# Performance work log

Hardware: AMD Instinct MI355X
Metric: run time of the kernel (lower is better)

Reference implementation:

```python
import jax, jax.numpy as jnp
import numpy as np

B, T, D = 4, 2048, 1024
H, S = 16, 64  # n_heads, stalk_dim; D == H*S
P_ADIC_BASE = 2
MAX_VAL = 16


def quantize_6bit(x):
    # symmetric int6 quantization with straight-through estimator
    scale = jnp.max(jnp.abs(x)) / 31.0 + 1e-8
    q = jnp.clip(jnp.round(x / scale), -31, 31) * scale
    return x + jax.lax.stop_gradient(q - x)


def build_p_adic_bias(seq_len, p=2, max_val=16):
    idx = jnp.arange(seq_len)
    d = jnp.abs(idx[:, None] - idx[None, :])
    nonzero = d > 0
    vp = jnp.zeros_like(d)
    work = d
    for _ in range(max_val):  # fixed iterations; v_2(|i-j|) <= log2(T) < 16
        divisible = nonzero & (work % p == 0)
        vp = vp + divisible.astype(vp.dtype)
        work = jnp.where(divisible, work // p, work)
    vals = jnp.minimum(vp, max_val).astype(jnp.float32)
    vals = jnp.where(nonzero, vals, jnp.float32(max_val))
    return vals / max_val


def setup_inputs() -> dict:
    key = jax.random.key(0)
    ks = jax.random.split(key, 8)
    std = 0.02
    return {
        "x": jax.random.normal(ks[0], (B, T, D), dtype=jnp.float32),
        "wq": jax.random.normal(ks[1], (D, D), dtype=jnp.float32) * std,
        "wk": jax.random.normal(ks[2], (D, D), dtype=jnp.float32) * std,
        "wv": jax.random.normal(ks[3], (D, D), dtype=jnp.float32) * std,
        "wo": jax.random.normal(ks[4], (D, D), dtype=jnp.float32) * std,
        "wu": jax.random.normal(ks[5], (S, S), dtype=jnp.float32) * std,
        "wsv": jax.random.normal(ks[6], (S, S), dtype=jnp.float32) * std,
        "p_scale": jnp.ones((1,), dtype=jnp.float32) * 0.1,
    }


def reference(x, wq, wk, wv, wo, wu, wsv, p_scale):
    h, s = H, S
    scale = 1.0 / jnp.sqrt(jnp.float32(s))
    # quantized linear projections (F.linear: x @ W.T)
    Q = (x @ quantize_6bit(wq).T).reshape(B, T, h, s).transpose(0, 2, 1, 3)
    K = (x @ quantize_6bit(wk).T).reshape(B, T, h, s).transpose(0, 2, 1, 3)
    V = (x @ quantize_6bit(wv).T).reshape(B, T, h, s).transpose(0, 2, 1, 3)
    # stalk (low-rank sheaf) maps on the head dim
    Qs = Q @ quantize_6bit(wu).T
    Ks = K @ quantize_6bit(wsv).T
    scores = jnp.einsum("bhqs,bhks->bhqk", Qs, Ks) * scale
    p_bias = build_p_adic_bias(T, p=P_ADIC_BASE, max_val=MAX_VAL)
    scores = scores + p_scale[0] * p_bias[None, None, :, :]
    causal = jnp.triu(jnp.ones((T, T), dtype=bool), k=1)
    scores = jnp.where(causal[None, None], -jnp.inf, scores)
    attn = jax.nn.softmax(scores, axis=-1)
    out = jnp.einsum("bhqk,bhks->bhqs", attn, V)
    out = out.transpose(0, 2, 1, 3).reshape(B, T, D)
    return out @ quantize_6bit(wo).T
```

## Files before the change

### kernel.cpp

```cpp
#include <hip/hip_runtime.h>
#include <hip/hip_bf16.h>
#include <stdint.h>


typedef __bf16 bf16_t;
typedef __attribute__((ext_vector_type(8))) __bf16 bf16x8;
typedef __attribute__((ext_vector_type(4))) float f32x4;

#define BB 4
#define TT 2048
#define DD 1024
#define HH 16
#define SS 64

__device__ __forceinline__ float quant6(float v, float s) {
    float q = rintf(v / s);
    q = fminf(fmaxf(q, -31.0f), 31.0f);
    return q * s;
}

__device__ __forceinline__ float fexp2(float x) {
#if __has_builtin(__builtin_amdgcn_exp2f)
    return __builtin_amdgcn_exp2f(x);
#else
    return exp2f(x);
#endif
}

typedef __attribute__((address_space(3))) uint32_t lds_u32;
typedef const __attribute__((address_space(1))) uint32_t glb_u32;

__global__ __launch_bounds__(256) void absmax6(const float* __restrict__ wq,
                                               const float* __restrict__ wk,
                                               const float* __restrict__ wv,
                                               const float* __restrict__ wo,
                                               const float* __restrict__ wu,
                                               const float* __restrict__ wsv,
                                               float* __restrict__ amax) {
    const int t = blockIdx.y;
    const float* src = (t == 0) ? wq : (t == 1) ? wk : (t == 2) ? wv
                     : (t == 3) ? wo : (t == 4) ? wu : wsv;
    const int n4 = (t < 4) ? (1048576 / 4) : (4096 / 4);
    float m = 0.0f;
    for (int i = blockIdx.x * blockDim.x + threadIdx.x; i < n4; i += gridDim.x * blockDim.x) {
        float4 v = ((const float4*)src)[i];
        m = fmaxf(m, fmaxf(fmaxf(fabsf(v.x), fabsf(v.y)), fmaxf(fabsf(v.z), fabsf(v.w))));
    }
    #pragma unroll
    for (int mask = 32; mask > 0; mask >>= 1)
        m = fmaxf(m, __shfl_xor(m, mask));
    __shared__ float red[4];
    int w = threadIdx.x >> 6;
    if ((threadIdx.x & 63) == 0) red[w] = m;
    __syncthreads();
    if (threadIdx.x == 0) {
        m = fmaxf(fmaxf(red[0], red[1]), fmaxf(red[2], red[3]));
        atomicMax((int*)(amax + t), __float_as_int(m));
    }
}

__global__ __launch_bounds__(256) void xcvt_kernel(const float* __restrict__ x,
                                                   bf16_t* __restrict__ xb) {
    int i = (blockIdx.x * 256 + threadIdx.x) * 8;
    float4 f0 = *(const float4*)(x + i);
    float4 f1 = *(const float4*)(x + i + 4);
    bf16x8 v;
    v[0] = (bf16_t)f0.x; v[1] = (bf16_t)f0.y; v[2] = (bf16_t)f0.z; v[3] = (bf16_t)f0.w;
    v[4] = (bf16_t)f1.x; v[5] = (bf16_t)f1.y; v[6] = (bf16_t)f1.z; v[7] = (bf16_t)f1.w;
    *(bf16x8*)(xb + i) = v;
}

__global__ __launch_bounds__(256) void quant_cast2(const float* __restrict__ wv,
                                                   const float* __restrict__ wo,
                                                   const float* __restrict__ amax,
                                                   bf16_t* __restrict__ dv,
                                                   bf16_t* __restrict__ dw) {
    const int which = blockIdx.y;
    const float* src = which ? wo : wv;
    bf16_t* dst = which ? dw : dv;
    float s = amax[which ? 3 : 2] / 31.0f + 1e-8f;
    int i = (blockIdx.x * 256 + threadIdx.x) * 8;
    float4 f0 = *(const float4*)(src + i);
    float4 f1 = *(const float4*)(src + i + 4);
    bf16x8 v;
    v[0] = (bf16_t)quant6(f0.x, s); v[1] = (bf16_t)quant6(f0.y, s);
    v[2] = (bf16_t)quant6(f0.z, s); v[3] = (bf16_t)quant6(f0.w, s);
    v[4] = (bf16_t)quant6(f1.x, s); v[5] = (bf16_t)quant6(f1.y, s);
    v[6] = (bf16_t)quant6(f1.z, s); v[7] = (bf16_t)quant6(f1.w, s);
    *(bf16x8*)(dst + i) = v;
}

__global__ __launch_bounds__(256) void fold_mfma(const float* __restrict__ wq,
                                                 const float* __restrict__ wk,
                                                 const float* __restrict__ wu,
                                                 const float* __restrict__ wsv,
                                                 const float* __restrict__ amax,
                                                 bf16_t* __restrict__ W_all) {
    const int which = blockIdx.y;
    const float* wbig = which ? wk : wq;
    const float* wsml = which ? wsv : wu;
    const float sb = amax[which ? 1 : 0] / 31.0f + 1e-8f;
    const float ss = amax[which ? 5 : 4] / 31.0f + 1e-8f;
    const float oscale = which ? 1.0f : 0.125f * 1.44269504089f;
    bf16_t* outp = W_all + (size_t)which * 1024 * 1024;
    const int h = blockIdx.x >> 4, n0 = (blockIdx.x & 15) * 64;
    const int w = threadIdx.x >> 6, l = threadIdx.x & 63;
    const int l15 = l & 15, quad = l >> 4, q8 = quad * 8;
    const int m0 = w * 16;

    bf16x8 af[2];
    #pragma unroll
    for (int kc = 0; kc < 2; ++kc) {
        const float* src = wsml + (m0 + l15) * 64 + kc * 32 + q8;
        float4 f0 = *(const float4*)(src);
        float4 f1 = *(const float4*)(src + 4);
        bf16x8 a;
        a[0] = (bf16_t)quant6(f0.x, ss); a[1] = (bf16_t)quant6(f0.y, ss);
        a[2] = (bf16_t)quant6(f0.z, ss); a[3] = (bf16_t)quant6(f0.w, ss);
        a[4] = (bf16_t)quant6(f1.x, ss); a[5] = (bf16_t)quant6(f1.y, ss);
        a[6] = (bf16_t)quant6(f1.z, ss); a[7] = (bf16_t)quant6(f1.w, ss);
        af[kc] = a;
    }
    f32x4 acc[4];
    #pragma unroll
    for (int nb = 0; nb < 4; ++nb) acc[nb] = (f32x4){0.f, 0.f, 0.f, 0.f};
    #pragma unroll
    for (int kc = 0; kc < 2; ++kc) {
        #pragma unroll
        for (int nb = 0; nb < 4; ++nb) {
            bf16x8 bfr;
            #pragma unroll
            for (int j = 0; j < 8; ++j)
                bfr[j] = (bf16_t)quant6(wbig[(size_t)(h * 64 + kc * 32 + q8 + j) * 1024 + n0 + nb * 16 + l15], sb);
            acc[nb] = __builtin_amdgcn_mfma_f32_16x16x32_bf16(af[kc], bfr, acc[nb], 0, 0, 0);
        }
    }
    #pragma unroll
    for (int nb = 0; nb < 4; ++nb)
        #pragma unroll
        for (int r = 0; r < 4; ++r)
            outp[(size_t)(h * 64 + m0 + quad * 4 + r) * 1024 + n0 + nb * 16 + l15] =
                (bf16_t)(acc[nb][r] * oscale);
}

template <bool OUT_F32>
__global__ __launch_bounds__(256) void gemm128(const bf16_t* __restrict__ A,
                                               const bf16_t* __restrict__ Bt,
                                               void* __restrict__ Cv,
                                               int lda, int ldb, int ldc, int K) {
    __shared__ __align__(16) bf16_t As[128 * 64];
    __shared__ __align__(16) bf16_t Bs[128 * 64];
    const int tid = threadIdx.x;
    const int w = tid >> 6, l = tid & 63;
    const int l15 = l & 15, quad = l >> 4;
    const int m0 = blockIdx.y * 128, n0 = blockIdx.x * 128;
    const int wm = (w & 1) * 64, wn = (w >> 1) * 64;

    f32x4 acc[4][4];
    #pragma unroll
    for (int a = 0; a < 4; ++a)
        #pragma unroll
        for (int b = 0; b < 4; ++b) acc[a][b] = (f32x4){0.f, 0.f, 0.f, 0.f};

    for (int kc = 0; kc < K; kc += 64) {
        __syncthreads();
        #pragma unroll
        for (int rep = 0; rep < 4; ++rep) {
            int ci = rep * 256 + w * 64 + l;
            int row = ci >> 3, slot = ci & 7;
            int gch = slot ^ ((row ^ (row >> 3)) & 7);
            __builtin_amdgcn_global_load_lds(
                (glb_u32*)(A + (size_t)(m0 + row) * lda + kc + gch * 8),
                (lds_u32*)(As + (rep * 256 + w * 64) * 8), 16, 0, 0);
            __builtin_amdgcn_global_load_lds(
                (glb_u32*)(Bt + (size_t)(n0 + row) * ldb + kc + gch * 8),
                (lds_u32*)(Bs + (rep * 256 + w * 64) * 8), 16, 0, 0);
        }
        __syncthreads();
        #pragma unroll
        for (int kb = 0; kb < 2; ++kb) {
            bf16x8 af[4], bfr[4];
            #pragma unroll
            for (int mb = 0; mb < 4; ++mb) {
                int row = wm + mb * 16 + l15;
                int slot = ((kb << 2) + quad) ^ ((row ^ (row >> 3)) & 7);
                af[mb] = *(const bf16x8*)(As + (row << 6) + slot * 8);
            }
            #pragma unroll
            for (int nb = 0; nb < 4; ++nb) {
                int row = wn + nb * 16 + l15;
                int slot = ((kb << 2) + quad) ^ ((row ^ (row >> 3)) & 7);
                bfr[nb] = *(const bf16x8*)(Bs + (row << 6) + slot * 8);
            }
            #pragma unroll
            for (int mb = 0; mb < 4; ++mb)
                #pragma unroll
                for (int nb = 0; nb < 4; ++nb)
                    acc[mb][nb] = __builtin_amdgcn_mfma_f32_16x16x32_bf16(af[mb], bfr[nb], acc[mb][nb], 0, 0, 0);
        }
    }
    #pragma unroll
    for (int mb = 0; mb < 4; ++mb) {
        #pragma unroll
        for (int nb = 0; nb < 4; ++nb) {
            int col = n0 + wn + nb * 16 + l15;
            #pragma unroll
            for (int r = 0; r < 4; ++r) {
                int row = m0 + wm + mb * 16 + quad * 4 + r;
                if constexpr (OUT_F32)
                    ((float*)Cv)[(size_t)row * ldc + col] = acc[mb][nb][r];
                else
                    ((bf16_t*)Cv)[(size_t)row * ldc + col] = (bf16_t)acc[mb][nb][r];
            }
        }
    }
}

__global__ __launch_bounds__(256) void vtrans_kernel(const bf16_t* __restrict__ QKV,
                                                     bf16_t* __restrict__ Vt) {
    __shared__ __align__(16) bf16_t tile[64 * 72];
    const int tid = threadIdx.x;
    const int bh = blockIdx.x >> 5, tt = blockIdx.x & 31;
    const int b = bh >> 4, h = bh & 15;
    #pragma unroll
    for (int rep = 0; rep < 2; ++rep) {
        int ci = rep * 256 + tid;
        int row = ci >> 3, ch = ci & 7;
        bf16x8 v = *(const bf16x8*)(QKV + ((size_t)(b * TT + tt * 64 + row)) * 3072 + 2048 + h * 64 + ch * 8);
        #pragma unroll
        for (int j = 0; j < 8; ++j) tile[(ch * 8 + j) * 72 + row] = v[j];
    }
    __syncthreads();
    #pragma unroll
    for (int rep = 0; rep < 2; ++rep) {
        int ci = rep * 256 + tid;
        int s = ci >> 3, ch = ci & 7;
        bf16x8 v = *(const bf16x8*)(tile + s * 72 + ch * 8);
        *(bf16x8*)(Vt + ((size_t)(bh * 64 + s)) * TT + tt * 64 + ch * 8) = v;
    }
}

__device__ __forceinline__ void attn_step(bf16_t* __restrict__ Pw, int rsel,
                                          const bf16x8 kb[4][2], const bf16x8 vb[4][2],
                                          const bf16x8 qa[2],
                                          f32x4* oacc, float* lrun,
                                          int q0, int kbase, bool diag, float pb2,
                                          int l15, int quad) {
    f32x4 sacc[4];
    #pragma unroll
    for (int c = 0; c < 4; ++c) sacc[c] = (f32x4){0.f, 0.f, 0.f, 0.f};
    #pragma unroll
    for (int kc = 0; kc < 2; ++kc)
        #pragma unroll
        for (int c = 0; c < 4; ++c)
            sacc[c] = __builtin_amdgcn_mfma_f32_16x16x32_bf16(qa[kc], kb[c][kc], sacc[c], 0, 0, 0);

    const int qr0 = q0 + quad * 4;
    #pragma unroll
    for (int c = 0; c < 4; ++c) {
        const int k = kbase + c * 16 + l15;
        const int ch = c * 2 + (l15 >> 3);
        #pragma unroll
        for (int r = 0; r < 4; ++r) {
            const int q = qr0 + r;
            const int d = q - k;
            float ctzf = (float)__builtin_ctz((unsigned)d | 0x10000u);
            float s2 = sacc[c][r] + pb2 * ctzf;
            if (diag && k > q) s2 = -INFINITY;
            float p = fexp2(s2);
            lrun[r] += p;
            int prow = rsel * 16 + quad * 4 + r;
            int slot = ch ^ ((prow ^ (prow >> 3)) & 7);
            Pw[prow * 64 + slot * 8 + (l15 & 7)] = (bf16_t)p;
        }
    }
    __builtin_amdgcn_wave_barrier();
    #pragma unroll
    for (int kc = 0; kc < 2; ++kc) {
        int prow = rsel * 16 + l15;
        int pslot = (kc * 4 + quad) ^ ((prow ^ (prow >> 3)) & 7);
        bf16x8 pa = *(const bf16x8*)(Pw + prow * 64 + pslot * 8);
        #pragma unroll
        for (int sb = 0; sb < 4; ++sb)
            oacc[sb] = __builtin_amdgcn_mfma_f32_16x16x32_bf16(pa, vb[sb][kc], oacc[sb], 0, 0, 0);
    }
    __builtin_amdgcn_wave_barrier();
}

__global__ __launch_bounds__(256, 2) void attn_kernel(const bf16_t* __restrict__ QKV,
                                                      const bf16_t* __restrict__ Vt,
                                                      const float* __restrict__ p_scale_ptr,
                                                      bf16_t* __restrict__ O) {
    __shared__ __align__(16) bf16_t Ks[64 * 64];
    __shared__ __align__(16) bf16_t Vs[64 * 64];
    __shared__ __align__(16) bf16_t Ps[4 * 32 * 64];

    const int tid = threadIdx.x;
    const int w = tid >> 6, l = tid & 63;
    const int l15 = l & 15, quad = l >> 4, q8 = quad * 8;
    const int pair = (blockIdx.x >> 3) & 15;
    const int bh = (blockIdx.x & 7) + ((blockIdx.x >> 7) << 3);
    const int b = bh >> 4, h = bh & 15;
    const int qtA = pair, qtB = 31 - pair;
    const int q0A = qtA * 64 + w * 16, q0B = qtB * 64 + w * 16;

    const float pb2 = p_scale_ptr[0] * 1.44269504089f * 0.0625f;
    const size_t xbase = (size_t)b * TT * 3072;

    bf16x8 qaA[2], qaB[2];
    #pragma unroll
    for (int kc = 0; kc < 2; ++kc) {
        qaA[kc] = *(const bf16x8*)(QKV + xbase + (size_t)(q0A + l15) * 3072 + h * 64 + kc * 32 + q8);
        qaB[kc] = *(const bf16x8*)(QKV + xbase + (size_t)(q0B + l15) * 3072 + h * 64 + kc * 32 + q8);
    }

    f32x4 oA[4], oB[4];
    float lA[4], lB[4];
    #pragma unroll
    for (int i = 0; i < 4; ++i) {
        oA[i] = (f32x4){0.f, 0.f, 0.f, 0.f};
        oB[i] = (f32x4){0.f, 0.f, 0.f, 0.f};
        lA[i] = 0.f; lB[i] = 0.f;
    }
    bf16_t* Pw = Ps + w * 2048;

    for (int kt = 0; kt <= qtB; ++kt) {
        const int kbase = kt * 64;
        __syncthreads();
        #pragma unroll
        for (int rep = 0; rep < 2; ++rep) {
            int ci = rep * 256 + tid;
            int row = ci >> 3, slot = ci & 7;
            int gch = slot ^ ((row ^ (row >> 3)) & 7);
            __builtin_amdgcn_global_load_lds(
                (glb_u32*)(QKV + xbase + (size_t)(kbase + row) * 3072 + 1024 + h * 64 + gch * 8),
                (lds_u32*)(Ks + (rep * 256 + w * 64) * 8), 16, 0, 0);
            __builtin_amdgcn_global_load_lds(
                (glb_u32*)(Vt + (size_t)bh * 131072 + (size_t)row * 2048 + kbase + gch * 8),
                (lds_u32*)(Vs + (rep * 256 + w * 64) * 8), 16, 0, 0);
        }
        __syncthreads();
        bf16x8 kb[4][2], vb[4][2];
        #pragma unroll
        for (int kc = 0; kc < 2; ++kc) {
            #pragma unroll
            for (int c = 0; c < 4; ++c) {
                int row = c * 16 + l15;
                int slot = (kc * 4 + quad) ^ ((row ^ (row >> 3)) & 7);
                kb[c][kc] = *(const bf16x8*)(Ks + row * 64 + slot * 8);
                vb[c][kc] = *(const bf16x8*)(Vs + row * 64 + slot * 8);
            }
        }
        attn_step(Pw, 1, kb, vb, qaB, oB, lB, q0B, kbase, kt == qtB, pb2, l15, quad);
        if (kt <= qtA)
            attn_step(Pw, 0, kb, vb, qaA, oA, lA, q0A, kbase, kt == qtA, pb2, l15, quad);
    }

    #pragma unroll
    for (int t = 0; t < 2; ++t) {
        float* lr = t ? lB : lA;
        f32x4* oo = t ? oB : oA;
        int q0 = t ? q0B : q0A;
        float inv[4];
        #pragma unroll
        for (int r = 0; r < 4; ++r) {
            float s = lr[r];
            s += __shfl_xor(s, 1); s += __shfl_xor(s, 2);
            s += __shfl_xor(s, 4); s += __shfl_xor(s, 8);
            inv[r] = 1.0f / s;
        }
        #pragma unroll
        for (int sb = 0; sb < 4; ++sb) {
            #pragma unroll
            for (int r = 0; r < 4; ++r) {
                int q = q0 + quad * 4 + r;
                int col = h * 64 + sb * 16 + l15;
                O[(size_t)(b * TT + q) * DD + col] = (bf16_t)(oo[sb][r] * inv[r]);
            }
        }
    }
}

extern "C" void kernel_launch(void* const* d_in, const int* in_sizes, int n_in,
                              void* d_out, int out_size, void* d_ws, size_t ws_size,
                              hipStream_t stream) {
    const float* x   = (const float*)d_in[0];
    const float* wq  = (const float*)d_in[1];
    const float* wk  = (const float*)d_in[2];
    const float* wv  = (const float*)d_in[3];
    const float* wo  = (const float*)d_in[4];
    const float* wu  = (const float*)d_in[5];
    const float* wsv = (const float*)d_in[6];
    const float* psc = (const float*)d_in[7];
    float* out = (float*)d_out;

    char* ws = (char*)d_ws;
    float*  amax  = (float*)(ws);
    bf16_t* W_all = (bf16_t*)(ws + 256);
    bf16_t* Wo    = (bf16_t*)(ws + 6291712);
    bf16_t* xb    = (bf16_t*)(ws + 8388864);
    bf16_t* Obuf  = xb;
    bf16_t* QKV   = (bf16_t*)(ws + 25166080);
    bf16_t* Vt    = (bf16_t*)(ws + 75497728);

    hipLaunchKernelGGL(absmax6, dim3(64, 6), dim3(256), 0, stream, wq, wk, wv, wo, wu, wsv, amax);
    hipLaunchKernelGGL(quant_cast2, dim3(512, 2), dim3(256), 0, stream,
                       wv, wo, amax, W_all + (size_t)2048 * 1024, Wo);
    hipLaunchKernelGGL(fold_mfma, dim3(256, 2), dim3(256), 0, stream, wq, wk, wu, wsv, amax, W_all);
    hipLaunchKernelGGL(xcvt_kernel, dim3(4096), dim3(256), 0, stream, x, xb);

    hipLaunchKernelGGL((gemm128<false>), dim3(24, 64), dim3(256), 0, stream,
                       xb, W_all, (void*)QKV, 1024, 1024, 3072, 1024);

    hipLaunchKernelGGL(vtrans_kernel, dim3(2048), dim3(256), 0, stream, QKV, Vt);

    hipLaunchKernelGGL(attn_kernel, dim3(1024), dim3(256), 0, stream, QKV, Vt, psc, Obuf);

    hipLaunchKernelGGL((gemm128<true>), dim3(8, 64), dim3(256), 0, stream,
                       Obuf, Wo, (void*)out, 1024, 1024, 1024, 1024);
}
```

Before: 297.3 us.

## Transpose attention score MFMA, halve P scratch, raise occupancy, merge weight-prep kernels

The score MFMA now computes K·Q instead of Q·K, so each lane owns a single query column. The running row sum collapses to one scalar per lane, and P is written as packed bf16x4 into a per-wave 16-row LDS buffer that is half the previous size. The smaller LDS and register footprint lets the launch bounds go from 2 to 4 blocks per CU. Separately, the quant_cast2 and fold_mfma weight-prep kernels are merged into a single prep_w launch to save a kernel launch. The risk is register spilling under the tighter launch bound, plus a different LDS bank pattern for the P writes.

```diff
diff --git a/kernel.cpp b/kernel.cpp
--- a/kernel.cpp
+++ b/kernel.cpp
@@ -4,6 +4,7 @@
 
 
 typedef __bf16 bf16_t;
+typedef __attribute__((ext_vector_type(4))) __bf16 bf16x4;
 typedef __attribute__((ext_vector_type(8))) __bf16 bf16x8;
 typedef __attribute__((ext_vector_type(4))) float f32x4;
 
@@ -70,40 +71,39 @@
     *(bf16x8*)(xb + i) = v;
 }
 
-__global__ __launch_bounds__(256) void quant_cast2(const float* __restrict__ wv,
-                                                   const float* __restrict__ wo,
-                                                   const float* __restrict__ amax,
-                                                   bf16_t* __restrict__ dv,
-                                                   bf16_t* __restrict__ dw) {
+__global__ __launch_bounds__(256) void prep_w(const float* __restrict__ wq,
+                                              const float* __restrict__ wk,
+                                              const float* __restrict__ wv,
+                                              const float* __restrict__ wo,
+                                              const float* __restrict__ wu,
+                                              const float* __restrict__ wsv,
+                                              const float* __restrict__ amax,
+                                              bf16_t* __restrict__ W_all,
+                                              bf16_t* __restrict__ Wo) {
     const int which = blockIdx.y;
-    const float* src = which ? wo : wv;
-    bf16_t* dst = which ? dw : dv;
-    float s = amax[which ? 3 : 2] / 31.0f + 1e-8f;
-    int i = (blockIdx.x * 256 + threadIdx.x) * 8;
-    float4 f0 = *(const float4*)(src + i);
-    float4 f1 = *(const float4*)(src + i + 4);
-    bf16x8 v;
-    v[0] = (bf16_t)quant6(f0.x, s); v[1] = (bf16_t)quant6(f0.y, s);
-    v[2] = (bf16_t)quant6(f0.z, s); v[3] = (bf16_t)quant6(f0.w, s);
-    v[4] = (bf16_t)quant6(f1.x, s); v[5] = (bf16_t)quant6(f1.y, s);
-    v[6] = (bf16_t)quant6(f1.z, s); v[7] = (bf16_t)quant6(f1.w, s);
-    *(bf16x8*)(dst + i) = v;
-}
-
-__global__ __launch_bounds__(256) void fold_mfma(const float* __restrict__ wq,
-                                                 const float* __restrict__ wk,
-                                                 const float* __restrict__ wu,
-                                                 const float* __restrict__ wsv,
-                                                 const float* __restrict__ amax,
-                                                 bf16_t* __restrict__ W_all) {
-    const int which = blockIdx.y;
+    if (blockIdx.x < 512) {
+        const float* src = which ? wo : wv;
+        bf16_t* dst = which ? Wo : (W_all + (size_t)2048 * 1024);
+        float s = amax[which ? 3 : 2] / 31.0f + 1e-8f;
+        int i = (blockIdx.x * 256 + threadIdx.x) * 8;
+        float4 f0 = *(const float4*)(src + i);
+        float4 f1 = *(const float4*)(src + i + 4);
+        bf16x8 v;
+        v[0] = (bf16_t)quant6(f0.x, s); v[1] = (bf16_t)quant6(f0.y, s);
+        v[2] = (bf16_t)quant6(f0.z, s); v[3] = (bf16_t)quant6(f0.w, s);
+        v[4] = (bf16_t)quant6(f1.x, s); v[5] = (bf16_t)quant6(f1.y, s);
+        v[6] = (bf16_t)quant6(f1.z, s); v[7] = (bf16_t)quant6(f1.w, s);
+        *(bf16x8*)(dst + i) = v;
+        return;
+    }
+    const int fx = blockIdx.x - 512;
     const float* wbig = which ? wk : wq;
     const float* wsml = which ? wsv : wu;
     const float sb = amax[which ? 1 : 0] / 31.0f + 1e-8f;
     const float ss = amax[which ? 5 : 4] / 31.0f + 1e-8f;
     const float oscale = which ? 1.0f : 0.125f * 1.44269504089f;
     bf16_t* outp = W_all + (size_t)which * 1024 * 1024;
-    const int h = blockIdx.x >> 4, n0 = (blockIdx.x & 15) * 64;
+    const int h = fx >> 4, n0 = (fx & 15) * 64;
     const int w = threadIdx.x >> 6, l = threadIdx.x & 63;
     const int l15 = l & 15, quad = l >> 4, q8 = quad * 8;
     const int m0 = w * 16;
@@ -240,11 +240,11 @@
     }
 }
 
-__device__ __forceinline__ void attn_step(bf16_t* __restrict__ Pw, int rsel,
+__device__ __forceinline__ void attn_step(bf16_t* __restrict__ Pw,
                                           const bf16x8 kb[4][2], const bf16x8 vb[4][2],
                                           const bf16x8 qa[2],
-                                          f32x4* oacc, float* lrun,
-                                          int q0, int kbase, bool diag, float pb2,
+                                          f32x4* oacc, float& lrun,
+                                          int qlane, int kbase, bool diag, float pb2,
                                           int l15, int quad) {
     f32x4 sacc[4];
     #pragma unroll
@@ -253,33 +253,30 @@
     for (int kc = 0; kc < 2; ++kc)
         #pragma unroll
         for (int c = 0; c < 4; ++c)
-            sacc[c] = __builtin_amdgcn_mfma_f32_16x16x32_bf16(qa[kc], kb[c][kc], sacc[c], 0, 0, 0);
-
-    const int qr0 = q0 + quad * 4;
+            sacc[c] = __builtin_amdgcn_mfma_f32_16x16x32_bf16(kb[c][kc], qa[kc], sacc[c], 0, 0, 0);
+
+    const int kp0 = kbase + quad * 4;
     #pragma unroll
     for (int c = 0; c < 4; ++c) {
-        const int k = kbase + c * 16 + l15;
-        const int ch = c * 2 + (l15 >> 3);
+        bf16x4 pk;
         #pragma unroll
         for (int r = 0; r < 4; ++r) {
-            const int q = qr0 + r;
-            const int d = q - k;
+            const int k = kp0 + c * 16 + r;
+            const int d = qlane - k;
             float ctzf = (float)__builtin_ctz((unsigned)d | 0x10000u);
             float s2 = sacc[c][r] + pb2 * ctzf;
-            if (diag && k > q) s2 = -INFINITY;
+            if (diag && k > qlane) s2 = -INFINITY;
             float p = fexp2(s2);
-            lrun[r] += p;
-            int prow = rsel * 16 + quad * 4 + r;
-            int slot = ch ^ ((prow ^ (prow >> 3)) & 7);
-            Pw[prow * 64 + slot * 8 + (l15 & 7)] = (bf16_t)p;
-        }
+            lrun += p;
+            pk[r] = (bf16_t)p;
+        }
+        int pp = (c * 2 + (quad >> 1)) ^ (l15 & 7);
+        *(bf16x4*)(Pw + l15 * 64 + pp * 8 + (quad & 1) * 4) = pk;
     }
     __builtin_amdgcn_wave_barrier();
     #pragma unroll
     for (int kc = 0; kc < 2; ++kc) {
-        int prow = rsel * 16 + l15;
-        int pslot = (kc * 4 + quad) ^ ((prow ^ (prow >> 3)) & 7);
-        bf16x8 pa = *(const bf16x8*)(Pw + prow * 64 + pslot * 8);
+        bf16x8 pa = *(const bf16x8*)(Pw + l15 * 64 + (((kc * 4 + quad) ^ (l15 & 7)) * 8));
         #pragma unroll
         for (int sb = 0; sb < 4; ++sb)
             oacc[sb] = __builtin_amdgcn_mfma_f32_16x16x32_bf16(pa, vb[sb][kc], oacc[sb], 0, 0, 0);
@@ -287,13 +284,13 @@
     __builtin_amdgcn_wave_barrier();
 }
 
-__global__ __launch_bounds__(256, 2) void attn_kernel(const bf16_t* __restrict__ QKV,
+__global__ __launch_bounds__(256, 4) void attn_kernel(const bf16_t* __restrict__ QKV,
                                                       const bf16_t* __restrict__ Vt,
                                                       const float* __restrict__ p_scale_ptr,
                                                       bf16_t* __restrict__ O) {
     __shared__ __align__(16) bf16_t Ks[64 * 64];
     __shared__ __align__(16) bf16_t Vs[64 * 64];
-    __shared__ __align__(16) bf16_t Ps[4 * 32 * 64];
+    __shared__ __align__(16) bf16_t Ps[4 * 16 * 64];
 
     const int tid = threadIdx.x;
     const int w = tid >> 6, l = tid & 63;
@@ -303,6 +300,7 @@
     const int b = bh >> 4, h = bh & 15;
     const int qtA = pair, qtB = 31 - pair;
     const int q0A = qtA * 64 + w * 16, q0B = qtB * 64 + w * 16;
+    const int qlA = q0A + l15, qlB = q0B + l15;
 
     const float pb2 = p_scale_ptr[0] * 1.44269504089f * 0.0625f;
     const size_t xbase = (size_t)b * TT * 3072;
@@ -315,14 +313,13 @@
     }
 
     f32x4 oA[4], oB[4];
-    float lA[4], lB[4];
+    float lA = 0.f, lB = 0.f;
     #pragma unroll
     for (int i = 0; i < 4; ++i) {
         oA[i] = (f32x4){0.f, 0.f, 0.f, 0.f};
         oB[i] = (f32x4){0.f, 0.f, 0.f, 0.f};
-        lA[i] = 0.f; lB[i] = 0.f;
-    }
-    bf16_t* Pw = Ps + w * 2048;
+    }
+    bf16_t* Pw = Ps + w * 1024;
 
     for (int kt = 0; kt <= qtB; ++kt) {
         const int kbase = kt * 64;
@@ -351,31 +348,27 @@
                 vb[c][kc] = *(const bf16x8*)(Vs + row * 64 + slot * 8);
             }
         }
-        attn_step(Pw, 1, kb, vb, qaB, oB, lB, q0B, kbase, kt == qtB, pb2, l15, quad);
+        attn_step(Pw, kb, vb, qaB, oB, lB, qlB, kbase, kt == qtB, pb2, l15, quad);
         if (kt <= qtA)
-            attn_step(Pw, 0, kb, vb, qaA, oA, lA, q0A, kbase, kt == qtA, pb2, l15, quad);
+            attn_step(Pw, kb, vb, qaA, oA, lA, qlA, kbase, kt == qtA, pb2, l15, quad);
     }
 
     #pragma unroll
     for (int t = 0; t < 2; ++t) {
-        float* lr = t ? lB : lA;
+        float s = t ? lB : lA;
         f32x4* oo = t ? oB : oA;
         int q0 = t ? q0B : q0A;
-        float inv[4];
+        s += __shfl_xor(s, 16);
+        s += __shfl_xor(s, 32);
+        float inv = 1.0f / s;
         #pragma unroll
         for (int r = 0; r < 4; ++r) {
-            float s = lr[r];
-            s += __shfl_xor(s, 1); s += __shfl_xor(s, 2);
-            s += __shfl_xor(s, 4); s += __shfl_xor(s, 8);
-            inv[r] = 1.0f / s;
-        }
-        #pragma unroll
-        for (int sb = 0; sb < 4; ++sb) {
-            #pragma unroll
-            for (int r = 0; r < 4; ++r) {
+            float invr = __shfl(inv, quad * 4 + r);
+            #pragma unroll
+            for (int sb = 0; sb < 4; ++sb) {
                 int q = q0 + quad * 4 + r;
                 int col = h * 64 + sb * 16 + l15;
-                O[(size_t)(b * TT + q) * DD + col] = (bf16_t)(oo[sb][r] * inv[r]);
+                O[(size_t)(b * TT + q) * DD + col] = (bf16_t)(oo[sb][r] * invr);
             }
         }
     }
@@ -404,9 +397,8 @@
     bf16_t* Vt    = (bf16_t*)(ws + 75497728);
 
     hipLaunchKernelGGL(absmax6, dim3(64, 6), dim3(256), 0, stream, wq, wk, wv, wo, wu, wsv, amax);
-    hipLaunchKernelGGL(quant_cast2, dim3(512, 2), dim3(256), 0, stream,
-                       wv, wo, amax, W_all + (size_t)2048 * 1024, Wo);
-    hipLaunchKernelGGL(fold_mfma, dim3(256, 2), dim3(256), 0, stream, wq, wk, wu, wsv, amax, W_all);
+    hipLaunchKernelGGL(prep_w, dim3(768, 2), dim3(256), 0, stream,
+                       wq, wk, wv, wo, wu, wsv, amax, W_all, Wo);
     hipLaunchKernelGGL(xcvt_kernel, dim3(4096), dim3(256), 0, stream, x, xb);
 
     hipLaunchKernelGGL((gemm128<false>), dim3(24, 64), dim3(256), 0, stream,
```

New measurement: 457.5 us. +53.9%, slower.
